# Kernel optimization log

Hardware: AMD Instinct MI355X
Metric: run time of the kernel (lower is better)

The kernel has to match this reference:

```python
import jax, jax.numpy as jnp
import numpy as np

B, T, L, D, H = 4, 1024, 1024, 1024, 16
HS = D // H          # head_size = 64
ROT = HS // 2        # rotary_ndims = 32


def setup_inputs() -> dict:
    key = jax.random.key(0)
    ks = jax.random.split(key, 8)
    x = jax.random.normal(ks[0], (B, T, D), dtype=jnp.float32)
    memory = jax.random.normal(ks[1], (B, L, D), dtype=jnp.float32)
    # RotaryEmbedding(rotary_ndims): inv_freq over ROT/2 freqs, emb = cat(freqs, freqs)
    inv_freq = 1.0 / (10000.0 ** (np.arange(0, ROT, 2, dtype=np.float32) / ROT))
    t = np.arange(T, dtype=np.float32)
    freqs = np.einsum('i,j->ij', t, inv_freq)            # [T, ROT/2]
    emb = np.concatenate([freqs, freqs], axis=-1)        # [T, ROT]
    RoPE = jnp.asarray(np.stack([np.cos(emb), np.sin(emb)]), dtype=jnp.float32)  # [2, T, ROT]
    s = 0.02
    Wq = jax.random.normal(ks[2], (D, D), dtype=jnp.float32) * s
    Wk = jax.random.normal(ks[3], (D, D), dtype=jnp.float32) * s
    Wv = jax.random.normal(ks[4], (D, D), dtype=jnp.float32) * s
    Wo = jax.random.normal(ks[5], (D, D), dtype=jnp.float32) * s
    bq = jnp.zeros((D,), jnp.float32)
    bk = jnp.zeros((D,), jnp.float32)
    bv = jnp.zeros((D,), jnp.float32)
    bo = jnp.zeros((D,), jnp.float32)
    return {"x": x, "memory": memory, "RoPE": RoPE,
            "Wq": Wq, "bq": bq, "Wk": Wk, "bk": bk,
            "Wv": Wv, "bv": bv, "Wo": Wo, "bo": bo}


def _rotate_half(u):
    u1, u2 = u[..., : u.shape[-1] // 2], u[..., u.shape[-1] // 2:]
    return jnp.concatenate([-u2, u1], axis=-1)


def _heads(y, n):  # [B, N, D] -> [B, H, N, HS]
    b = y.shape[0]
    return y.reshape(b, n, H, HS).transpose(0, 2, 1, 3)


def _attn(q, k, v):
    scale = 1.0 / jnp.sqrt(jnp.asarray(k.shape[-1], q.dtype))
    att = jnp.einsum('bhtd,bhsd->bhts', q, k) * scale
    att = jax.nn.softmax(att, axis=-1)
    return jnp.einsum('bhts,bhsd->bhtd', att, v)


def reference(x, memory, RoPE, Wq, bq, Wk, bk, Wv, bv, Wo, bo):
    b, t, d = x.shape
    l = memory.shape[1]
    cos, sin = RoPE[0][:t], RoPE[1][:t]  # [T, ROT], broadcasts over [B,H,T,ROT]

    # ---- self-attention with partial rotary ----
    q = _heads(x @ Wq.T + bq, t)
    k = _heads(x @ Wk.T + bk, t)
    v = _heads(x @ Wv.T + bv, t)
    q_rot, q_pass = q[..., :ROT], q[..., ROT:]
    k_rot, k_pass = k[..., :ROT], k[..., ROT:]
    q_rot = q_rot * cos + _rotate_half(q_rot) * sin
    k_rot = k_rot * cos + _rotate_half(k_rot) * sin
    q = jnp.concatenate([q_rot, q_pass], axis=-1)
    k = jnp.concatenate([k_rot, k_pass], axis=-1)
    y = _attn(q, k, v)                                   # [B,H,T,HS]
    y = y.transpose(0, 2, 1, 3).reshape(b, t, d)

    # ---- cross-attention (no rotary) ----
    q = _heads(y @ Wq.T + bq, t)
    k = _heads(memory @ Wk.T + bk, l)
    v = _heads(memory @ Wv.T + bv, l)
    y = _attn(q, k, v)
    y = y.transpose(0, 2, 1, 3).reshape(b, t, d)
    return y @ Wo.T + bo
```

## Files before the change

kernel.cpp:

```cpp
#include <hip/hip_runtime.h>

typedef unsigned short u16;
typedef __attribute__((ext_vector_type(8))) unsigned short ushort8;
typedef __attribute__((ext_vector_type(4))) unsigned short ushort4v;
typedef __attribute__((ext_vector_type(4))) float f32x4;
typedef __bf16 bf16x8 __attribute__((ext_vector_type(8)));


__device__ __forceinline__ u16 f2bf(float f) {
    unsigned u = __builtin_bit_cast(unsigned, f);
    unsigned r = u + 0x7fffu + ((u >> 16) & 1u);
    return (u16)(r >> 16);
}

typedef const __attribute__((address_space(1))) unsigned gu32;
typedef __attribute__((address_space(3))) unsigned lu32;
__device__ __forceinline__ void gload16(const void* g, void* l) {
    __builtin_amdgcn_global_load_lds((gu32*)g, (lu32*)l, 16, 0, 0);
}

__device__ __forceinline__ float dpp_sum16(float x) {
    int v = __builtin_bit_cast(int, x);
    x += __builtin_bit_cast(float, __builtin_amdgcn_update_dpp(0, v, 0xB1, 0xF, 0xF, true));
    v = __builtin_bit_cast(int, x);
    x += __builtin_bit_cast(float, __builtin_amdgcn_update_dpp(0, v, 0x4E, 0xF, 0xF, true));
    v = __builtin_bit_cast(int, x);
    x += __builtin_bit_cast(float, __builtin_amdgcn_update_dpp(0, v, 0x141, 0xF, 0xF, true));
    v = __builtin_bit_cast(int, x);
    x += __builtin_bit_cast(float, __builtin_amdgcn_update_dpp(0, v, 0x140, 0xF, 0xF, true));
    return x;
}

__global__ void k_f2b(const float4* __restrict__ in, u16* __restrict__ out, int n4) {
    int i = blockIdx.x * blockDim.x + threadIdx.x;
    if (i >= n4) return;
    float4 v = in[i];
    ushort4v r = { f2bf(v.x), f2bf(v.y), f2bf(v.z), f2bf(v.w) };
    *(ushort4v*)(out + (size_t)i * 4) = r;
}

__global__ void k_f2bw(const float4* __restrict__ a0, const float4* __restrict__ a1,
                       const float4* __restrict__ a2, const float4* __restrict__ a3,
                       u16* __restrict__ o0, u16* __restrict__ o1,
                       u16* __restrict__ o2, u16* __restrict__ o3) {
    int wsel = blockIdx.x >> 10;
    const float4* in = wsel == 0 ? a0 : wsel == 1 ? a1 : wsel == 2 ? a2 : a3;
    u16* out = wsel == 0 ? o0 : wsel == 1 ? o1 : wsel == 2 ? o2 : o3;
    int i = (blockIdx.x & 1023) * 256 + threadIdx.x;
    float4 v = in[i];
    ushort4v r = { f2bf(v.x), f2bf(v.y), f2bf(v.z), f2bf(v.w) };
    *(ushort4v*)(out + (size_t)i * 4) = r;
}

template<int NSEG, int OUTBF, int ROPE, int VTOUT, int QS>
__global__ __launch_bounds__(256) void k_gemm(
        const u16* __restrict__ a0, const u16* __restrict__ a1, const u16* __restrict__ a2,
        const u16* __restrict__ w0, const u16* __restrict__ w1, const u16* __restrict__ w2,
        const float* __restrict__ b0, const float* __restrict__ b1, const float* __restrict__ b2,
        const float* __restrict__ ropep,
        void* __restrict__ Cp, u16* __restrict__ VTo, int ldc) {
    __shared__ ushort8 sA[2][512];
    __shared__ ushort8 sB[2][512];
    const int tid = threadIdx.x, lane = tid & 63, w = tid >> 6;
    const int wr = w >> 1, wc = w & 1;

    const int nbx = gridDim.x;
    const int orig = blockIdx.y * nbx + blockIdx.x;
    const int qq = (nbx * gridDim.y) >> 3;
    const int logical = (orig & 7) * qq + (orig >> 3);
    const int bx = logical % nbx;
    const int m0 = (logical / nbx) * 128;

    int seg = 0;
    if (NSEG >= 2 && bx >= 8)  seg = 1;
    if (NSEG >= 3 && bx >= 16) seg = 2;
    const u16* Ap = seg == 0 ? a0 : seg == 1 ? a1 : a2;
    const u16* W  = seg == 0 ? w0 : seg == 1 ? w1 : w2;
    const float* bias = seg == 0 ? b0 : seg == 1 ? b1 : b2;
    const int n0w = (bx & 7) * 128;
    const int outc0 = bx * 128;
    const int isV = VTOUT && (seg == NSEG - 1);
    const float ls = (QS && seg == 0) ? 0.18033688011112042f : 1.0f;

    f32x4 acc[4][4] = {};

    const u16* asrc = Ap + (size_t)(m0 + 32 * w + (lane & 15)) * 1024 + (lane >> 4) * 8;
    const u16* bsrc = W  + (size_t)(n0w + 32 * w + (lane & 15)) * 1024 + (lane >> 4) * 8;

#define G_STAGE(p, kt) do { \
    gload16(asrc + (kt),             &sA[p][w * 128]); \
    gload16(asrc + (kt) + 16 * 1024, &sA[p][w * 128 + 64]); \
    gload16(bsrc + (kt),             &sB[p][w * 128]); \
    gload16(bsrc + (kt) + 16 * 1024, &sB[p][w * 128 + 64]); } while (0)

#define G_COMPUTE(p) do { \
    bf16x8 af[4], bfr[4]; \
    for (int i = 0; i < 4; i++) af[i]  = __builtin_bit_cast(bf16x8, sA[p][(wr * 4 + i) * 64 + lane]); \
    for (int j = 0; j < 4; j++) bfr[j] = __builtin_bit_cast(bf16x8, sB[p][(wc * 4 + j) * 64 + lane]); \
    for (int i = 0; i < 4; i++) \
        for (int j = 0; j < 4; j++) \
            acc[i][j] = __builtin_amdgcn_mfma_f32_16x16x32_bf16(af[i], bfr[j], acc[i][j], 0, 0, 0); } while (0)

    G_STAGE(0, 0);
    __syncthreads();
    for (int t = 0; t < 30; t += 2) {
        G_STAGE(1, (t + 1) * 32);
        G_COMPUTE(0);
        __syncthreads();
        G_STAGE(0, (t + 2) * 32);
        G_COMPUTE(1);
        __syncthreads();
    }
    G_STAGE(1, 31 * 32);
    G_COMPUTE(0);
    __syncthreads();
    G_COMPUTE(1);
#undef G_STAGE
#undef G_COMPUTE

    const int er = (lane >> 4) * 4, ec = lane & 15;
    if (isV) {
        for (int i = 0; i < 4; i++) {
            int srow = m0 + wr * 64 + i * 16 + er;
            int bb = srow >> 10, s0 = srow & 1023;
            for (int j = 0; j < 4; j++) {
                int gcolV = n0w + wc * 64 + j * 16 + ec;
                int hh = gcolV >> 6, dd = gcolV & 63;
                float bia = bias[gcolV];
                ushort4v pk;
                for (int e = 0; e < 4; e++) pk[e] = f2bf(acc[i][j][e] + bia);
                *(ushort4v*)(VTo + (size_t)((bb * 16 + hh) * 64 + dd) * 1024 + s0) = pk;
            }
        }
    } else if (ROPE) {
        const float* cosp = ropep;
        const float* sinp = ropep + 32768;
        for (int i = 0; i < 4; i++) {
            int grow_base = m0 + wr * 64 + i * 16 + er;
            float bv0 = bias[n0w + wc * 64 + ec];
            float bv1 = bias[n0w + wc * 64 + 16 + ec];
            float bv2 = bias[n0w + wc * 64 + 32 + ec];
            float bv3 = bias[n0w + wc * 64 + 48 + ec];
            for (int e = 0; e < 4; e++) {
                int grow = grow_base + e;
                int t = grow & 1023;
                float c = cosp[t * 32 + ec];
                float s = sinp[t * 32 + ec];
                float v0 = acc[i][0][e] + bv0;
                float v1 = acc[i][1][e] + bv1;
                u16* row = (u16*)Cp + (size_t)grow * ldc + outc0 + wc * 64 + ec;
                row[0]  = f2bf((v0 * c - v1 * s) * ls);
                row[16] = f2bf((v1 * c + v0 * s) * ls);
                row[32] = f2bf((acc[i][2][e] + bv2) * ls);
                row[48] = f2bf((acc[i][3][e] + bv3) * ls);
            }
        }
    } else {
        for (int i = 0; i < 4; i++) {
            int grow_base = m0 + wr * 64 + i * 16 + er;
            for (int j = 0; j < 4; j++) {
                int cl = wc * 64 + j * 16 + ec;
                float bia = bias[n0w + cl];
                int gcol = outc0 + cl;
                for (int e = 0; e < 4; e++) {
                    float v = (acc[i][j][e] + bia) * ls;
                    if (OUTBF) ((u16*)Cp)[(size_t)(grow_base + e) * ldc + gcol] = f2bf(v);
                    else       ((float*)Cp)[(size_t)(grow_base + e) * ldc + gcol] = v;
                }
            }
        }
    }
}

__global__ __launch_bounds__(256) void k_attn(const u16* __restrict__ Q, const u16* __restrict__ K,
                                              const u16* __restrict__ VTb, u16* __restrict__ O) {
    __shared__ ushort8 sK[2][512];
    __shared__ ushort8 sV[2][512];
    __shared__ ushort8 sP[512];

    const int tid = threadIdx.x, lane = tid & 63, w = tid >> 6;
    const int n = blockIdx.x + (blockIdx.y << 4) + (blockIdx.z << 8);
    const int sl = n >> 3;
    const int bh = ((n & 7) << 3) | (sl & 7);
    const int qt = sl >> 3;
    const int b = bh >> 4, h = bh & 15;

    const u16* Qh = Q + (size_t)(b * 1024 + qt * 64) * 2048 + h * 64;
    const u16* Kh = K + (size_t)(b * 1024) * 2048 + h * 64;
    const u16* VTh = VTb + (size_t)(bh * 64) * 1024;

    const u16* qa = Qh + (size_t)(16 * w + (lane & 15)) * 2048 + (lane >> 4) * 8;
    bf16x8 qf0 = __builtin_bit_cast(bf16x8, *(const ushort8*)qa);
    bf16x8 qf1 = __builtin_bit_cast(bf16x8, *(const ushort8*)(qa + 32));

    float lsum[4] = { 0.f, 0.f, 0.f, 0.f };
    f32x4 o[4] = {};

    const int mrow = (lane >> 4) * 4;
    const int hi8 = (lane & 15) >> 3;
    const int se7 = lane & 7;

    const u16* ks = Kh + (size_t)(16 * w + (lane & 15)) * 2048 + (lane >> 4) * 8;
    const u16* vs = VTh + (size_t)(16 * w + (lane & 15)) * 1024 + (lane >> 4) * 8;

#define A_STAGE(p, s0) do { \
    gload16(ks + (size_t)(s0) * 2048,        &sK[p][w * 128]); \
    gload16(ks + (size_t)((s0) + 32) * 2048, &sK[p][w * 128 + 64]); \
    gload16(vs + (s0),                       &sV[p][w * 128]); \
    gload16(vs + (s0) + 32,                  &sV[p][w * 128 + 64]); } while (0)

#define A_COMPUTE(p) do { \
    f32x4 sfr[4]; \
    for (int cb = 0; cb < 4; cb++) { \
        bf16x8 k0 = __builtin_bit_cast(bf16x8, sK[p][cb * 128 + lane]); \
        bf16x8 k1 = __builtin_bit_cast(bf16x8, sK[p][cb * 128 + 64 + lane]); \
        f32x4 a = {}; \
        a = __builtin_amdgcn_mfma_f32_16x16x32_bf16(qf0, k0, a, 0, 0, 0); \
        a = __builtin_amdgcn_mfma_f32_16x16x32_bf16(qf1, k1, a, 0, 0, 0); \
        sfr[cb] = a; \
    } \
    u16* sPw = ((u16*)sP) + w * 1024; \
    for (int cb = 0; cb < 4; cb++) { \
        int schunk = cb * 2 + hi8; \
        int cbase = (schunk >> 2) * 64 + (schunk & 3) * 16; \
        for (int e = 0; e < 4; e++) { \
            float pv = __builtin_amdgcn_exp2f(sfr[cb][e]); \
            lsum[e] += pv; \
            int ch = cbase + mrow + e; \
            ch ^= (ch >> 3) & 7; \
            sPw[ch * 8 + se7] = __builtin_bit_cast(u16, (__bf16)pv); \
        } \
    } \
    int c0 = lane ^ ((lane >> 3) & 7); \
    int c1 = (64 + lane) ^ (((64 + lane) >> 3) & 7); \
    bf16x8 pf0 = __builtin_bit_cast(bf16x8, sP[w * 128 + c0]); \
    bf16x8 pf1 = __builtin_bit_cast(bf16x8, sP[w * 128 + c1]); \
    for (int db = 0; db < 4; db++) { \
        bf16x8 v0 = __builtin_bit_cast(bf16x8, sV[p][db * 128 + lane]); \
        bf16x8 v1 = __builtin_bit_cast(bf16x8, sV[p][db * 128 + 64 + lane]); \
        o[db] = __builtin_amdgcn_mfma_f32_16x16x32_bf16(pf0, v0, o[db], 0, 0, 0); \
        o[db] = __builtin_amdgcn_mfma_f32_16x16x32_bf16(pf1, v1, o[db], 0, 0, 0); \
    } } while (0)

    A_STAGE(0, 0);
    __syncthreads();
    for (int t = 0; t < 14; t += 2) {
        A_STAGE(1, (t + 1) * 64);
        A_COMPUTE(0);
        __syncthreads();
        A_STAGE(0, (t + 2) * 64);
        A_COMPUTE(1);
        __syncthreads();
    }
    A_STAGE(1, 15 * 64);
    A_COMPUTE(0);
    __syncthreads();
    A_COMPUTE(1);
#undef A_STAGE
#undef A_COMPUTE

    float rcp[4];
    for (int e = 0; e < 4; e++) rcp[e] = 1.0f / dpp_sum16(lsum[e]);
    for (int db = 0; db < 4; db++) {
        int gcol = h * 64 + db * 16 + (lane & 15);
        for (int e = 0; e < 4; e++) {
            int grow = qt * 64 + 16 * w + mrow + e;
            O[(size_t)(b * 1024 + grow) * 1024 + gcol] = f2bf(o[db][e] * rcp[e]);
        }
    }
}

extern "C" void kernel_launch(void* const* d_in, const int* in_sizes, int n_in,
                              void* d_out, int out_size, void* d_ws, size_t ws_size,
                              hipStream_t stream) {
    const float* x    = (const float*)d_in[0];
    const float* mem  = (const float*)d_in[1];
    const float* rope = (const float*)d_in[2];
    const float* Wq   = (const float*)d_in[3];
    const float* bq   = (const float*)d_in[4];
    const float* Wk   = (const float*)d_in[5];
    const float* bk   = (const float*)d_in[6];
    const float* Wv   = (const float*)d_in[7];
    const float* bv   = (const float*)d_in[8];
    const float* Wo   = (const float*)d_in[9];
    const float* bo   = (const float*)d_in[10];
    float* out = (float*)d_out;

    char* ws = (char*)d_ws;
    const size_t MB = 1024 * 1024;
    u16* wqb = (u16*)(ws + 0 * MB);
    u16* wkb = (u16*)(ws + 2 * MB);
    u16* wvb = (u16*)(ws + 4 * MB);
    u16* wob = (u16*)(ws + 6 * MB);
    u16* QKV = (u16*)(ws + 8 * MB);
    u16* VT  = (u16*)(ws + 24 * MB);
    u16* SH  = (u16*)(ws + 32 * MB);
    u16* memb = (u16*)d_out;

    k_f2bw<<<4096, 256, 0, stream>>>((const float4*)Wq, (const float4*)Wk,
                                     (const float4*)Wv, (const float4*)Wo,
                                     wqb, wkb, wvb, wob);
    k_f2b<<<4096, 256, 0, stream>>>((const float4*)x, SH, 1048576);
    k_gemm<3, 1, 1, 1, 1><<<dim3(24, 32), 256, 0, stream>>>(
        SH, SH, SH, wqb, wkb, wvb, bq, bk, bv, rope, QKV, VT, 2048);
    k_attn<<<dim3(16, 16, 4), 256, 0, stream>>>(QKV, QKV + 1024, VT, SH);

    k_f2b<<<4096, 256, 0, stream>>>((const float4*)mem, memb, 1048576);
    k_gemm<3, 1, 0, 1, 1><<<dim3(24, 32), 256, 0, stream>>>(
        SH, memb, memb, wqb, wkb, wvb, bq, bk, bv, nullptr, QKV, VT, 2048);
    k_attn<<<dim3(16, 16, 4), 256, 0, stream>>>(QKV, QKV + 1024, VT, SH);

    k_gemm<1, 0, 0, 0, 0><<<dim3(8, 32), 256, 0, stream>>>(
        SH, SH, SH, wob, wob, wob, bo, bo, bo, nullptr, out, nullptr, 1024);
}
```

Baseline: 363.9 us.

## Split-K output projection with atomics and separate V transpose kernel

```diff
diff --git a/kernel.cpp b/kernel.cpp
--- a/kernel.cpp
+++ b/kernel.cpp
@@ -52,13 +52,13 @@
     *(ushort4v*)(out + (size_t)i * 4) = r;
 }
 
-template<int NSEG, int OUTBF, int ROPE, int VTOUT, int QS>
+template<int NSEG, int OUTBF, int ROPE, int QS, int VSEP, int KSPLIT>
 __global__ __launch_bounds__(256) void k_gemm(
         const u16* __restrict__ a0, const u16* __restrict__ a1, const u16* __restrict__ a2,
         const u16* __restrict__ w0, const u16* __restrict__ w1, const u16* __restrict__ w2,
         const float* __restrict__ b0, const float* __restrict__ b1, const float* __restrict__ b2,
         const float* __restrict__ ropep,
-        void* __restrict__ Cp, u16* __restrict__ VTo, int ldc) {
+        void* __restrict__ Cp, u16* __restrict__ Vp, int ldc) {
     __shared__ ushort8 sA[2][512];
     __shared__ ushort8 sB[2][512];
     const int tid = threadIdx.x, lane = tid & 63, w = tid >> 6;
@@ -69,7 +69,11 @@
     const int qq = (nbx * gridDim.y) >> 3;
     const int logical = (orig & 7) * qq + (orig >> 3);
     const int bx = logical % nbx;
-    const int m0 = (logical / nbx) * 128;
+    const int mi = logical / nbx;
+    const int kh = KSPLIT ? (mi & 1) : 0;
+    const int m0 = (KSPLIT ? (mi >> 1) : mi) * 128;
+    const int kbeg = kh * 512;
+    const int NIT = KSPLIT ? 16 : 32;
 
     int seg = 0;
     if (NSEG >= 2 && bx >= 8)  seg = 1;
@@ -79,13 +83,13 @@
     const float* bias = seg == 0 ? b0 : seg == 1 ? b1 : b2;
     const int n0w = (bx & 7) * 128;
     const int outc0 = bx * 128;
-    const int isV = VTOUT && (seg == NSEG - 1);
+    const int isV = VSEP && (seg == NSEG - 1);
     const float ls = (QS && seg == 0) ? 0.18033688011112042f : 1.0f;
 
     f32x4 acc[4][4] = {};
 
-    const u16* asrc = Ap + (size_t)(m0 + 32 * w + (lane & 15)) * 1024 + (lane >> 4) * 8;
-    const u16* bsrc = W  + (size_t)(n0w + 32 * w + (lane & 15)) * 1024 + (lane >> 4) * 8;
+    const u16* asrc = Ap + (size_t)(m0 + 32 * w + (lane & 15)) * 1024 + kbeg + (lane >> 4) * 8;
+    const u16* bsrc = W  + (size_t)(n0w + 32 * w + (lane & 15)) * 1024 + kbeg + (lane >> 4) * 8;
 
 #define G_STAGE(p, kt) do { \
     gload16(asrc + (kt),             &sA[p][w * 128]); \
@@ -103,7 +107,7 @@
 
     G_STAGE(0, 0);
     __syncthreads();
-    for (int t = 0; t < 30; t += 2) {
+    for (int t = 0; t + 2 < NIT; t += 2) {
         G_STAGE(1, (t + 1) * 32);
         G_COMPUTE(0);
         __syncthreads();
@@ -111,7 +115,7 @@
         G_COMPUTE(1);
         __syncthreads();
     }
-    G_STAGE(1, 31 * 32);
+    G_STAGE(1, (NIT - 1) * 32);
     G_COMPUTE(0);
     __syncthreads();
     G_COMPUTE(1);
@@ -119,17 +123,27 @@
 #undef G_COMPUTE
 
     const int er = (lane >> 4) * 4, ec = lane & 15;
-    if (isV) {
+    if (KSPLIT) {
+        float* of = (float*)Cp;
         for (int i = 0; i < 4; i++) {
-            int srow = m0 + wr * 64 + i * 16 + er;
-            int bb = srow >> 10, s0 = srow & 1023;
+            int grow_base = m0 + wr * 64 + i * 16 + er;
             for (int j = 0; j < 4; j++) {
-                int gcolV = n0w + wc * 64 + j * 16 + ec;
-                int hh = gcolV >> 6, dd = gcolV & 63;
-                float bia = bias[gcolV];
-                ushort4v pk;
-                for (int e = 0; e < 4; e++) pk[e] = f2bf(acc[i][j][e] + bia);
-                *(ushort4v*)(VTo + (size_t)((bb * 16 + hh) * 64 + dd) * 1024 + s0) = pk;
+                int cl = wc * 64 + j * 16 + ec;
+                float bia = (kh == 0) ? bias[n0w + cl] : 0.0f;
+                int gcol = outc0 + cl;
+                for (int e = 0; e < 4; e++)
+                    atomicAdd(&of[(size_t)(grow_base + e) * ldc + gcol], acc[i][j][e] + bia);
+            }
+        }
+    } else if (isV) {
+        const int vc0 = outc0 - (NSEG - 1) * 1024;
+        for (int i = 0; i < 4; i++) {
+            int grow_base = m0 + wr * 64 + i * 16 + er;
+            for (int j = 0; j < 4; j++) {
+                int cl = wc * 64 + j * 16 + ec;
+                float bia = bias[n0w + cl];
+                for (int e = 0; e < 4; e++)
+                    Vp[(size_t)(grow_base + e) * 1024 + vc0 + cl] = f2bf(acc[i][j][e] + bia);
             }
         }
     } else if (ROPE) {
@@ -169,6 +183,26 @@
                 }
             }
         }
+    }
+}
+
+__global__ __launch_bounds__(256) void k_vt(const u16* __restrict__ Vb, u16* __restrict__ VTo) {
+    __shared__ u16 tile[64][72];
+    const int tid = threadIdx.x, lane = tid & 63, w = tid >> 6;
+    const int sx = blockIdx.x, bh = blockIdx.y;
+    const int b = bh >> 4, h = bh & 15;
+    const u16* Vp = Vb + (size_t)(b * 1024 + sx * 64) * 1024 + h * 64;
+    for (int it = 0; it < 2; it++) {
+        int c = tid + it * 256, r = c >> 3, dc = c & 7;
+        *(ushort8*)&tile[r][dc * 8] = *(const ushort8*)(Vp + (size_t)r * 1024 + dc * 8);
+    }
+    __syncthreads();
+    u16* outp = VTo + (size_t)(bh * 64 + lane) * 1024 + sx * 64;
+    for (int it = 0; it < 2; it++) {
+        int sc = w + it * 4;
+        ushort8 tv;
+        for (int e = 0; e < 8; e++) tv[e] = tile[sc * 8 + e][lane];
+        *(ushort8*)(outp + sc * 8) = tv;
     }
 }
 
@@ -288,28 +322,32 @@
 
     char* ws = (char*)d_ws;
     const size_t MB = 1024 * 1024;
-    u16* wqb = (u16*)(ws + 0 * MB);
-    u16* wkb = (u16*)(ws + 2 * MB);
-    u16* wvb = (u16*)(ws + 4 * MB);
-    u16* wob = (u16*)(ws + 6 * MB);
-    u16* QKV = (u16*)(ws + 8 * MB);
-    u16* VT  = (u16*)(ws + 24 * MB);
-    u16* SH  = (u16*)(ws + 32 * MB);
+    u16* wqb  = (u16*)(ws + 0 * MB);
+    u16* wkb  = (u16*)(ws + 2 * MB);
+    u16* wvb  = (u16*)(ws + 4 * MB);
+    u16* wob  = (u16*)(ws + 6 * MB);
+    u16* QKV  = (u16*)(ws + 8 * MB);
+    u16* VT   = (u16*)(ws + 24 * MB);
+    u16* SH   = (u16*)(ws + 32 * MB);
+    u16* Vbuf = (u16*)(ws + 40 * MB);
     u16* memb = (u16*)d_out;
 
     k_f2bw<<<4096, 256, 0, stream>>>((const float4*)Wq, (const float4*)Wk,
                                      (const float4*)Wv, (const float4*)Wo,
                                      wqb, wkb, wvb, wob);
     k_f2b<<<4096, 256, 0, stream>>>((const float4*)x, SH, 1048576);
-    k_gemm<3, 1, 1, 1, 1><<<dim3(24, 32), 256, 0, stream>>>(
-        SH, SH, SH, wqb, wkb, wvb, bq, bk, bv, rope, QKV, VT, 2048);
+    k_gemm<3, 1, 1, 1, 1, 0><<<dim3(24, 32), 256, 0, stream>>>(
+        SH, SH, SH, wqb, wkb, wvb, bq, bk, bv, rope, QKV, Vbuf, 2048);
+    k_vt<<<dim3(16, 64), 256, 0, stream>>>(Vbuf, VT);
     k_attn<<<dim3(16, 16, 4), 256, 0, stream>>>(QKV, QKV + 1024, VT, SH);
 
     k_f2b<<<4096, 256, 0, stream>>>((const float4*)mem, memb, 1048576);
-    k_gemm<3, 1, 0, 1, 1><<<dim3(24, 32), 256, 0, stream>>>(
-        SH, memb, memb, wqb, wkb, wvb, bq, bk, bv, nullptr, QKV, VT, 2048);
+    k_gemm<3, 1, 0, 1, 1, 0><<<dim3(24, 32), 256, 0, stream>>>(
+        SH, memb, memb, wqb, wkb, wvb, bq, bk, bv, nullptr, QKV, Vbuf, 2048);
+    k_vt<<<dim3(16, 64), 256, 0, stream>>>(Vbuf, VT);
+    hipMemsetAsync(out, 0, (size_t)out_size * sizeof(float), stream);
     k_attn<<<dim3(16, 16, 4), 256, 0, stream>>>(QKV, QKV + 1024, VT, SH);
 
-    k_gemm<1, 0, 0, 0, 0><<<dim3(8, 32), 256, 0, stream>>>(
+    k_gemm<1, 0, 0, 0, 0, 1><<<dim3(8, 64), 256, 0, stream>>>(
         SH, SH, SH, wob, wob, wob, bo, bo, bo, nullptr, out, nullptr, 1024);
 }
```

Measured after the change: 388.3 us. +6.7%, slower.
